# Performance work log

Hardware: AMD Instinct MI355X
Metric: run time of the kernel (lower is better)

## Reference

```python
import jax, jax.numpy as jnp
import numpy as np

B, NF, G, H, W = 4, 64, 8, 96, 96
K, KK = 3, 9
CG = NF // G  # channels per deformable group


def _conv3(x, w, b):
    # 3x3 conv, stride 1, pad 1, NCHW/OIHW
    y = jax.lax.conv_general_dilated(x, w, (1, 1), ((1, 1), (1, 1)),
                                     dimension_numbers=('NCHW', 'OIHW', 'NCHW'))
    return y + b[None, :, None, None]


def _lrelu(x):
    return jnp.where(x >= 0, x, 0.1 * x)


def _up2(x):
    # bilinear x2 upsample, align_corners=False (PyTorch semantics: src clamped at 0, indices clamped at n-1)
    def up_axis(x, axis):
        n = x.shape[axis]
        src = jnp.maximum((jnp.arange(2 * n, dtype=jnp.float32) + 0.5) / 2.0 - 0.5, 0.0)
        i0 = jnp.floor(src).astype(jnp.int32)
        i1 = jnp.minimum(i0 + 1, n - 1)
        t = (src - i0.astype(jnp.float32))
        x0 = jnp.take(x, i0, axis=axis)
        x1 = jnp.take(x, i1, axis=axis)
        shp = [1] * x.ndim
        shp[axis] = 2 * n
        t = t.reshape(shp)
        return x0 * (1.0 - t) + x1 * t
    return up_axis(up_axis(x, 2), 3)


def _dcn(x, off_feat, w_om, b_om, w_d, b_d):
    # Modulated deformable conv (DCNv2, separate offset input), 3x3, stride 1, pad 1, dil 1,
    # conv groups = 1, deformable groups = G.
    b, c, h, w = x.shape
    om = _conv3(off_feat, w_om, b_om)                     # [B, 3*G*KK, H, W]
    o_y, o_x, m = jnp.split(om, 3, axis=1)                # each [B, G*KK, H, W]
    off_y = o_y.reshape(b, G, KK, h, w)
    off_x = o_x.reshape(b, G, KK, h, w)
    mask = jax.nn.sigmoid(m).reshape(b, G, KK, h, w)

    dy = (jnp.arange(KK, dtype=jnp.float32) // K - 1.0)   # [-1,-1,-1,0,0,0,1,1,1]
    dx = (jnp.arange(KK, dtype=jnp.float32) % K - 1.0)
    ys = jnp.arange(h, dtype=jnp.float32)
    xs = jnp.arange(w, dtype=jnp.float32)
    # sampling positions: [B, G, KK, H, W]
    py = off_y + ys[None, None, None, :, None] + dy[None, None, :, None, None]
    px = off_x + xs[None, None, None, None, :] + dx[None, None, :, None, None]

    y0f = jnp.floor(py); x0f = jnp.floor(px)
    ty = py - y0f; tx = px - x0f
    y0 = y0f.astype(jnp.int32); x0 = x0f.astype(jnp.int32)
    y1 = y0 + 1; x1 = x0 + 1

    xg = x.reshape(b, G, CG, h * w)  # per-deformable-group channels

    def samp(iy, ix):
        valid = ((iy >= 0) & (iy < h) & (ix >= 0) & (ix < w)).astype(x.dtype)  # [B,G,KK,H,W]
        idx = jnp.clip(iy, 0, h - 1) * w + jnp.clip(ix, 0, w - 1)
        idxf = idx.reshape(b, G, 1, KK * h * w)
        v = jnp.take_along_axis(xg, jnp.broadcast_to(idxf, (b, G, CG, KK * h * w)), axis=3)
        return v.reshape(b, G, CG, KK, h, w) * valid[:, :, None]

    w00 = ((1 - ty) * (1 - tx))[:, :, None]
    w01 = ((1 - ty) * tx)[:, :, None]
    w10 = (ty * (1 - tx))[:, :, None]
    w11 = (ty * tx)[:, :, None]
    cols = (samp(y0, x0) * w00 + samp(y0, x1) * w01 +
            samp(y1, x0) * w10 + samp(y1, x1) * w11)
    cols = cols * mask[:, :, None]                        # modulation
    cols = cols.reshape(b, c, KK, h, w)
    out = jnp.einsum('bckhw,ock->bohw', cols, w_d.reshape(c, c, KK))
    return out + b_d[None, :, None, None]


def setup_inputs() -> dict:
    key = jax.random.key(0)
    ks = jax.random.split(key, 20)
    s = 0.05
    inp = {
        'src0': jax.random.normal(ks[0], (B, NF, H, W), jnp.float32),
        'src1': jax.random.normal(ks[1], (B, NF, H, W), jnp.float32),
        'last_offset': jax.random.normal(ks[2], (B, NF, H // 2, W // 2), jnp.float32),
        'last_feature': jax.random.normal(ks[3], (B, NF, H // 2, W // 2), jnp.float32),
        'w_off1': jax.random.normal(ks[4], (NF, 2 * NF, 3, 3), jnp.float32) * s,
        'b_off1': jax.random.normal(ks[5], (NF,), jnp.float32) * s,
        'w_off2': jax.random.normal(ks[6], (NF, 2 * NF, 3, 3), jnp.float32) * s,
        'b_off2': jax.random.normal(ks[7], (NF,), jnp.float32) * s,
        'w_off3': jax.random.normal(ks[8], (NF, NF, 3, 3), jnp.float32) * s,
        'b_off3': jax.random.normal(ks[9], (NF,), jnp.float32) * s,
        'w_om': jax.random.normal(ks[10], (3 * G * KK, NF, 3, 3), jnp.float32) * s,
        'b_om': jax.random.normal(ks[11], (3 * G * KK,), jnp.float32) * s,
        'w_dcn': jax.random.normal(ks[12], (NF, NF, 3, 3), jnp.float32) * s,
        'b_dcn': jax.random.normal(ks[13], (NF,), jnp.float32) * s,
        'w_fea': jax.random.normal(ks[14], (NF, 2 * NF, 3, 3), jnp.float32) * s,
        'b_fea': jax.random.normal(ks[15], (NF,), jnp.float32) * s,
    }
    return inp


def reference(src0, src1, last_offset, last_feature,
              w_off1, b_off1, w_off2, b_off2, w_off3, b_off3,
              w_om, b_om, w_dcn, b_dcn, w_fea, b_fea):
    offset = _lrelu(_conv3(jnp.concatenate([src0, src1], axis=1), w_off1, b_off1))
    lo = _up2(last_offset)
    offset = _lrelu(_conv3(jnp.concatenate([offset, lo * 2.0], axis=1), w_off2, b_off2))
    offset = _lrelu(_conv3(offset, w_off3, b_off3))
    feature = _dcn(src0, offset, w_om, b_om, w_dcn, b_dcn)
    lf = _up2(last_feature)
    feature = _conv3(jnp.concatenate([feature, lf], axis=1), w_fea, b_fea)
    feature = _lrelu(feature)
    return (offset, feature)
```

## Files before the change

### kernel.cpp

```cpp
#include <hip/hip_runtime.h>
#include <hip/hip_fp16.h>
#include <math.h>

typedef __attribute__((ext_vector_type(8))) short bf16x8;
typedef __attribute__((ext_vector_type(8))) _Float16 half8;
typedef __attribute__((ext_vector_type(4))) float f32x4;
typedef __attribute__((ext_vector_type(4))) int int4v;

#define GL_LDS16(g, l) __builtin_amdgcn_global_load_lds( \
    (const __attribute__((address_space(1))) void*)(g), \
    (__attribute__((address_space(3))) void*)(l), 16, 0, 0)

__device__ __forceinline__ ushort f2bf(float f) {
    union { float f; unsigned u; } v; v.f = f;
    unsigned r = (v.u + 0x7fffu + ((v.u >> 16) & 1u)) >> 16;
    return (ushort)r;
}
__device__ __forceinline__ float bf2f(ushort h) {
    union { unsigned u; float f; } v; v.u = ((unsigned)h) << 16;
    return v.f;
}

__device__ __forceinline__ void prep_one(const float* __restrict__ w,
        ushort* __restrict__ wp, int u, int Cin, int CoutR, int CoutP) {
    int oc = u % CoutP; int t = u / CoutP;
    int kg = t & 3; t >>= 2;
    int kk = t % 9; int cc = t / 9;
    alignas(16) ushort tmp[8];
    for (int j = 0; j < 8; ++j) {
        int c = cc * 32 + kg * 8 + j;
        float v = (oc < CoutR) ? w[((size_t)oc * Cin + c) * 9 + kk] : 0.f;
        tmp[j] = f2bf(v);
    }
    *(int4v*)(wp + (size_t)u * 8) = *(int4v*)tmp;
}

__global__ __launch_bounds__(256) void pack_combo_k(
        const float* __restrict__ s0, const float* __restrict__ s1,
        const float* __restrict__ lo, const float* __restrict__ lf,
        const float* __restrict__ w1, const float* __restrict__ w2,
        const float* __restrict__ w3, const float* __restrict__ wom,
        const float* __restrict__ wd, const float* __restrict__ wf,
        const float* __restrict__ bom,
        ushort* __restrict__ xin1, ushort* __restrict__ xin2,
        ushort* __restrict__ xin4, ushort* __restrict__ xg1,
        ushort* __restrict__ w1p, ushort* __restrict__ w2p,
        ushort* __restrict__ w3p, ushort* __restrict__ womp,
        ushort* __restrict__ wdp, ushort* __restrict__ wfp,
        float* __restrict__ bpp, float* __restrict__ zg) {
    int b = blockIdx.y;
    int z = blockIdx.z;
    int px = blockIdx.x * 64 + (threadIdx.x & 63);
    int u = threadIdx.x >> 6;
    if (z == 0) {
        for (int half = 0; half < 2; ++half) {
            int cg = u + half * 4;
            float vals[16];
            alignas(16) ushort tmp[16];
            for (int i = 0; i < 16; ++i) {
                int c = cg * 16 + i;
                float v = (c < 64) ? s0[((size_t)(b * 64 + c)) * 9216 + px]
                                   : s1[((size_t)(b * 64 + c - 64)) * 9216 + px];
                vals[i] = v;
                tmp[i] = f2bf(v);
            }
            ushort* dst = xin1 + ((size_t)(b * 9216) + px) * 128 + cg * 16;
            *(int4v*)dst = *(int4v*)&tmp[0];
            *(int4v*)(dst + 8) = *(int4v*)&tmp[8];
            if (half == 0) {
                alignas(16) __half th[16];
                for (int i = 0; i < 16; ++i) th[i] = __float2half(vals[i]);
                ushort* gdst = xg1 + (((size_t)(b * 8 + cg * 2) * 9216) + px) * 8;
                *(int4v*)gdst = *(int4v*)&th[0];
                *(int4v*)(gdst + 9216 * 8) = *(int4v*)&th[8];
            }
        }
    } else if (z < 3) {
        const float* in = (z == 1) ? lo : lf;
        float scale = (z == 1) ? 2.0f : 1.0f;
        ushort* xo = (z == 1) ? xin2 : xin4;
        int y = px / 96, x = px % 96;
        float sy = fmaxf(y * 0.5f - 0.25f, 0.f);
        float sx = fmaxf(x * 0.5f - 0.25f, 0.f);
        int y0 = (int)sy, x0 = (int)sx;
        float ty = sy - (float)y0, tx = sx - (float)x0;
        int y1 = min(y0 + 1, 47), x1 = min(x0 + 1, 47);
        alignas(16) ushort tmp[16];
        for (int i = 0; i < 16; ++i) {
            int c = u * 16 + i;
            const float* p = in + ((size_t)(b * 64 + c)) * 2304;
            float v00 = p[y0 * 48 + x0], v01 = p[y0 * 48 + x1];
            float v10 = p[y1 * 48 + x0], v11 = p[y1 * 48 + x1];
            float v = (v00 * (1.f - tx) + v01 * tx) * (1.f - ty)
                    + (v10 * (1.f - tx) + v11 * tx) * ty;
            tmp[i] = f2bf(v * scale);
        }
        ushort* dst = xo + ((size_t)(b * 9216) + px) * 128 + 64 + u * 16;
        *(int4v*)dst = *(int4v*)&tmp[0];
        *(int4v*)(dst + 8) = *(int4v*)&tmp[8];
    } else {
        int uu = (blockIdx.x + 144 * blockIdx.y) * 256 + threadIdx.x;
        if (uu < 9216) prep_one(w1, w1p, uu, 128, 64, 64);
        else if (uu < 18432) prep_one(w2, w2p, uu - 9216, 128, 64, 64);
        else if (uu < 23040) prep_one(w3, w3p, uu - 18432, 64, 64, 64);
        else if (uu < 43776) {
            int v = uu - 23040;
            int ocp = v % 288; int t = v / 288;
            int kg = t & 3; t >>= 2;
            int kk = t % 9; int cc = t / 9;
            int t3 = ocp & 3, gkkp = ocp >> 2;
            alignas(16) ushort tmp[8];
            for (int j = 0; j < 8; ++j) {
                int c = cc * 32 + kg * 8 + j;
                float vv = (t3 < 3)
                    ? wom[((size_t)(t3 * 72 + gkkp) * 64 + c) * 9 + kk] : 0.f;
                tmp[j] = f2bf(vv);
            }
            *(int4v*)(womp + (size_t)v * 8) = *(int4v*)tmp;
        } else if (uu < 48384) {
            int v = uu - 43776;
            int oc = v & 63; int gkk = v >> 6;
            int g = gkk / 9, kk = gkk % 9;
            alignas(16) __half tmp[8];
            for (int j = 0; j < 8; ++j)
                tmp[j] = __float2half(wd[((size_t)oc * 64 + g * 8 + j) * 9 + kk]);
            *(int4v*)(wdp + (size_t)v * 8) = *(int4v*)tmp;
        } else if (uu < 57600) prep_one(wf, wfp, uu - 48384, 128, 64, 64);
        else if (uu < 57888) {
            int ocp = uu - 57600; int t3 = ocp & 3, gkkp = ocp >> 2;
            bpp[ocp] = (t3 < 3) ? bom[t3 * 72 + gkkp] : 0.f;
        } else if (uu < 57904) zg[uu - 57888] = 0.f;
    }
}

template<int CIN, int MT, int NZ, bool LRELU, bool ST_F32, bool ST_CHL>
__global__ __launch_bounds__(256, 4) void conv_mfma_k(
        const ushort* __restrict__ xin,
        const ushort* __restrict__ wp,
        const float* __restrict__ bias,
        float* __restrict__ outf,
        ushort* __restrict__ chl,
        const ushort* __restrict__ zg,
        int CoutR, int CoutP, int ochs, int ocoff) {
    constexpr int SL = CIN / 64;
    constexpr int OCN = MT * 16;
    __shared__ ushort s_act[SL][7200];

    int tid = threadIdx.x;
    int wv = tid >> 6, ln = tid & 63;
    int l15 = ln & 15, l4 = ln >> 4;

    constexpr int TOTAL = 144 * 4 * NZ;
    constexpr int CHUNK = TOTAL / 8;
    int bid = blockIdx.x;
    int nid = (bid & 7) * CHUNK + (bid >> 3);
    int zc = nid % NZ; int r1 = nid / NZ;
    int tile = r1 % 144; int b = r1 / 144;
    int bx = (tile % 12) * 8, by = (tile / 12) * 8;
    int oc0 = zc * OCN;

    int px_l = wv * 16 + l15;
    int py = px_l >> 3, pxx = px_l & 7;
    int b_base = (py * 10 + pxx) * 72 + l4 * 8;

    const ushort* wlane = wp + ((size_t)l4 * CoutP + oc0 + l15) * 8;

    f32x4 acc[MT];
#pragma unroll
    for (int mt = 0; mt < MT; ++mt) acc[mt] = (f32x4){0.f, 0.f, 0.f, 0.f};

    auto STAGE = [&](int sl, int buf) {
        for (int i = tid; i < 900; i += 256) {
            int p = i / 9, q = i - p * 9;
            int gy = by + (p / 10) - 1, gx = bx + (p % 10) - 1;
            const ushort* src = zg;
            if (q < 8 && (unsigned)gy < 96u && (unsigned)gx < 96u)
                src = xin + ((size_t)(b * 9216 + gy * 96 + gx) * CIN
                             + sl * 64 + q * 8);
            GL_LDS16(src, s_act[buf] + (size_t)i * 8);
        }
    };

    STAGE(0, 0);
    __syncthreads();
#pragma unroll
    for (int sl = 0; sl < SL; ++sl) {
        if (sl + 1 < SL) STAGE(sl + 1, (sl + 1) & 1);
#pragma unroll
        for (int cc2 = 0; cc2 < 2; ++cc2) {
#pragma unroll
            for (int kk = 0; kk < 9; ++kk) {
                bf16x8 bfrag = *(const bf16x8*)(s_act[sl & (SL - 1)] + b_base +
                                   ((kk / 3) * 10 + (kk % 3)) * 72 + cc2 * 32);
#pragma unroll
                for (int mt = 0; mt < MT; ++mt) {
                    bf16x8 af = *(const bf16x8*)(wlane +
                        ((size_t)((sl * 2 + cc2) * 36 + kk * 4) * CoutP + mt * 16) * 8);
                    acc[mt] = __builtin_amdgcn_mfma_f32_16x16x32_bf16(
                        af, bfrag, acc[mt], 0, 0, 0);
                }
            }
        }
        if (sl + 1 < SL) __syncthreads();
    }

    int gy = by + py, gx = bx + pxx;
    size_t pxg = (size_t)b * 9216 + gy * 96 + gx;
#pragma unroll
    for (int mt = 0; mt < MT; ++mt) {
        int ocb = oc0 + mt * 16 + l4 * 4;
        ushort hb[4];
#pragma unroll
        for (int r = 0; r < 4; ++r) {
            int oc = ocb + r;
            float v = acc[mt][r] + ((oc < CoutR) ? bias[oc] : 0.f);
            if (LRELU) v = (v >= 0.f) ? v : 0.1f * v;
            hb[r] = f2bf(v);
            if (ST_F32 && oc < CoutR)
                outf[((size_t)b * CoutR + oc) * 9216 + gy * 96 + gx] = v;
        }
        if (ST_CHL && ocb < CoutR) {
            uint2 pk;
            pk.x = (uint)hb[0] | ((uint)hb[1] << 16);
            pk.y = (uint)hb[2] | ((uint)hb[3] << 16);
            *(uint2*)(chl + pxg * ochs + ocoff + ocb) = pk;
        }
    }
}

__global__ __launch_bounds__(192, 2) void dcn_fused_k(
        const ushort* __restrict__ xoff,
        const ushort* __restrict__ xg1,
        const ushort* __restrict__ womp,
        const float* __restrict__ bpp,
        const ushort* __restrict__ wdp,
        const float* __restrict__ bd, ushort* __restrict__ chl,
        const ushort* __restrict__ zg) {
    __shared__ ushort s_x[3456];
    __shared__ float s_red[2][64][17];
    int tid = threadIdx.x;
    int kq = tid >> 6, ln = tid & 63;
    int l15 = ln & 15, l4 = ln >> 4;
    int bid = blockIdx.x;
    int nid = (bid & 7) * 288 + (bid >> 3);
    int pxb = nid % 576; int b = nid / 576;
    int px0 = pxb * 16;
    int px = px0 + l15;
    int y = px0 / 96, x0 = px0 % 96;
    int xx = x0 + l15;

    for (int i = tid; i < 432; i += 192) {
        int P = i >> 3, s8 = i & 7;
        int q = s8 ^ (P & 7);
        int ry = y - 1 + P / 18, rx = x0 - 1 + P % 18;
        const ushort* src = zg;
        if ((unsigned)ry < 96u && (unsigned)rx < 96u)
            src = xoff + (((size_t)b * 9216 + ry * 96 + rx) * 64 + q * 8);
        GL_LDS16(src, s_x + (size_t)i * 8);
    }
    __syncthreads();

    f32x4 acc[4];
#pragma unroll
    for (int mt = 0; mt < 4; ++mt) acc[mt] = (f32x4){0.f, 0.f, 0.f, 0.f};

    int4v Ab[3][4];
    float cwb[3][4];

    auto PREP = [&](int s, const f32x4& aom, int4v* A, float* cw) {
        int st = kq * 6 + s;
        int gkk = st * 4 + l4;
        int g = gkk / 9, kk = gkk - g * 9;
        int bofs = st * 16 + l4 * 4;
        float oy = aom[0] + bpp[bofs];
        float ox = aom[1] + bpp[bofs + 1];
        float mm = 1.f / (1.f + __expf(-(aom[2] + bpp[bofs + 2])));
        float py = oy + (float)(y + kk / 3 - 1);
        float pxf = ox + (float)(xx + kk % 3 - 1);
        float yf = floorf(py), xf = floorf(pxf);
        float fy = py - yf, fx = pxf - xf;
        int iy0 = (int)yf, ix0 = (int)xf;
        int iy1 = iy0 + 1, ix1 = ix0 + 1;
        float vy0 = ((unsigned)iy0 < 96u) ? 1.f : 0.f;
        float vy1 = ((unsigned)iy1 < 96u) ? 1.f : 0.f;
        float vx0 = ((unsigned)ix0 < 96u) ? 1.f : 0.f;
        float vx1 = ((unsigned)ix1 < 96u) ? 1.f : 0.f;
        int r0 = min(max(iy0, 0), 95), r1 = min(max(iy1, 0), 95);
        int lb = min(max(ix0, 0), 94);
        float h0 = (float)min(max(ix0 - lb, 0), 1);
        float h1 = (float)min(max(ix1 - lb, 0), 1);
        float wx0 = (1.f - fx) * vx0, wx1 = fx * vx1;
        float xw0 = wx0 * (1.f - h0) + wx1 * (1.f - h1);
        float xw1 = wx0 * h0 + wx1 * h1;
        float rw0 = (1.f - fy) * vy0 * mm, rw1 = fy * vy1 * mm;
        cw[0] = rw0 * xw0; cw[1] = rw0 * xw1;
        cw[2] = rw1 * xw0; cw[3] = rw1 * xw1;
        const ushort* gp = xg1 + ((size_t)(b * 8 + g) * 9216) * 8;
        const ushort* p0 = gp + ((size_t)(r0 * 96 + lb)) * 8;
        const ushort* p1 = gp + ((size_t)(r1 * 96 + lb)) * 8;
        A[0] = *(const int4v*)p0;
        A[1] = *(const int4v*)(p0 + 8);
        A[2] = *(const int4v*)p1;
        A[3] = *(const int4v*)(p1 + 8);
    };

    auto CONSUME = [&](int s, const int4v* A, const float* cw) {
        union { int4v v; __half2 h2[4]; } a0, a1, b0, b1;
        a0.v = A[0]; a1.v = A[1]; b0.v = A[2]; b1.v = A[3];
        __half2 w0 = __float2half2_rn(cw[0]);
        __half2 w1 = __float2half2_rn(cw[1]);
        __half2 w2 = __float2half2_rn(cw[2]);
        __half2 w3 = __float2half2_rn(cw[3]);
        union { __half2 h2[4]; half8 v; } bu;
#pragma unroll
        for (int j = 0; j < 4; ++j) {
            __half2 t = __hmul2(a0.h2[j], w0);
            t = __hfma2(a1.h2[j], w1, t);
            t = __hfma2(b0.h2[j], w2, t);
            t = __hfma2(b1.h2[j], w3, t);
            bu.h2[j] = t;
        }
        int gkk = (kq * 6 + s) * 4 + l4;
#pragma unroll
        for (int mt = 0; mt < 4; ++mt) {
            half8 af = *(const half8*)(wdp +
                ((size_t)gkk * 64 + mt * 16 + l15) * 8);
            acc[mt] = __builtin_amdgcn_mfma_f32_16x16x32_f16(
                af, bu.v, acc[mt], 0, 0, 0);
        }
    };

#pragma unroll
    for (int s = 0; s < 8; ++s) {
        if (s < 6) {
            f32x4 aom = (f32x4){0.f, 0.f, 0.f, 0.f};
#pragma unroll
            for (int kk = 0; kk < 9; ++kk) {
                int ky = kk / 3, kx = kk % 3;
#pragma unroll
                for (int cc = 0; cc < 2; ++cc) {
                    int P = ky * 18 + l15 + kx;
                    int c8 = cc * 4 + l4;
                    bf16x8 bfrag = *(const bf16x8*)(s_x +
                        ((size_t)(P * 8 + (c8 ^ (P & 7)))) * 8);
                    bf16x8 af = *(const bf16x8*)(womp +
                        ((size_t)(((cc * 9 + kk) * 4 + l4) * 288)
                         + (kq * 6 + s) * 16 + l15) * 8);
                    aom = __builtin_amdgcn_mfma_f32_16x16x32_bf16(
                        af, bfrag, aom, 0, 0, 0);
                }
            }
            PREP(s, aom, Ab[s % 3], cwb[s % 3]);
        }
        if (s >= 2) CONSUME(s - 2, Ab[(s - 2) % 3], cwb[(s - 2) % 3]);
    }

    if (kq) {
#pragma unroll
        for (int mt = 0; mt < 4; ++mt)
#pragma unroll
            for (int r = 0; r < 4; ++r)
                s_red[kq - 1][ln][mt * 4 + r] = acc[mt][r];
    }
    __syncthreads();
    if (!kq) {
        size_t pb = (size_t)b * 9216 + px;
#pragma unroll
        for (int mt = 0; mt < 4; ++mt) {
            ushort hb[4];
#pragma unroll
            for (int r = 0; r < 4; ++r) {
                int oc = mt * 16 + l4 * 4 + r;
                float v = acc[mt][r] + s_red[0][ln][mt * 4 + r]
                        + s_red[1][ln][mt * 4 + r] + bd[oc];
                hb[r] = f2bf(v);
            }
            uint2 pk;
            pk.x = (uint)hb[0] | ((uint)hb[1] << 16);
            pk.y = (uint)hb[2] | ((uint)hb[3] << 16);
            *(uint2*)(chl + pb * 128 + mt * 16 + l4 * 4) = pk;
        }
    }
}

extern "C" void kernel_launch(void* const* d_in, const int* in_sizes, int n_in,
                              void* d_out, int out_size, void* d_ws, size_t ws_size,
                              hipStream_t stream) {
    const float* src0  = (const float*)d_in[0];
    const float* src1  = (const float*)d_in[1];
    const float* l_off = (const float*)d_in[2];
    const float* l_fea = (const float*)d_in[3];
    const float* w1 = (const float*)d_in[4];   const float* b1 = (const float*)d_in[5];
    const float* w2 = (const float*)d_in[6];   const float* b2 = (const float*)d_in[7];
    const float* w3 = (const float*)d_in[8];   const float* b3 = (const float*)d_in[9];
    const float* wom = (const float*)d_in[10]; const float* bom = (const float*)d_in[11];
    const float* wd = (const float*)d_in[12];  const float* bd = (const float*)d_in[13];
    const float* wf = (const float*)d_in[14];  const float* bf = (const float*)d_in[15];

    char* W = (char*)d_ws;
    ushort* xin1 = (ushort*)(W + 0);
    ushort* xin2 = (ushort*)(W + 9437184);
    ushort* xoff = (ushort*)(W + 9437184);
    ushort* xin3 = (ushort*)(W + 18874368);
    ushort* xin4 = (ushort*)(W + 44826624);
    ushort* xg1  = (ushort*)(W + 54263808);
    ushort* w1p  = (ushort*)(W + 58982400);
    ushort* w2p  = (ushort*)(W + 59129856);
    ushort* w3p  = (ushort*)(W + 59277312);
    ushort* womp = (ushort*)(W + 59351040);
    ushort* wdp  = (ushort*)(W + 59682816);
    ushort* wfp  = (ushort*)(W + 59756544);
    float*  bpp  = (float*)(W + 59904000);
    float*  zgrd = (float*)(W + 59905152);

    float* out_off = (float*)d_out;
    float* out_fea = out_off + (size_t)4 * 64 * 9216;

    pack_combo_k<<<dim3(144, 4, 4), 256, 0, stream>>>(
        src0, src1, l_off, l_fea, w1, w2, w3, wom, wd, wf, bom,
        xin1, xin2, xin4, xg1, w1p, w2p, w3p, womp, wdp, wfp, bpp, zgrd);

    const ushort* zg = (const ushort*)zgrd;
    conv_mfma_k<128, 2, 2, true, false, true><<<1152, 256, 0, stream>>>(
        xin1, w1p, b1, nullptr, xin2, zg, 64, 64, 128, 0);
    conv_mfma_k<128, 2, 2, true, false, true><<<1152, 256, 0, stream>>>(
        xin2, w2p, b2, nullptr, xin3, zg, 64, 64, 64, 0);
    conv_mfma_k<64, 2, 2, true, true, true><<<1152, 256, 0, stream>>>(
        xin3, w3p, b3, out_off, xoff, zg, 64, 64, 64, 0);
    dcn_fused_k<<<2304, 192, 0, stream>>>(xoff, xg1, womp, bpp, wdp, bd,
                                          xin4, zg);
    conv_mfma_k<128, 2, 2, true, true, false><<<1152, 256, 0, stream>>>(
        xin4, wfp, bf, out_fea, nullptr, zg, 64, 64, 0, 0);
}
```

Baseline: 131.9 us.

## Process two 16-pixel groups per block in fused DCN kernel

Each block of the fused offset-conv plus deformable-conv kernel now covers 32 pixels instead of 16, with a wider shared-memory halo tile and a halved grid. The offset-mask and DCN weight fragments loaded from global memory are reused across two MFMA accumulator sets, which halves weight traffic per pixel and amortizes halo loads. The software pipeline changes from a 3-deep to a 2-deep buffer. This raises register and LDS use per block and may reduce occupancy or latency hiding.

```diff
diff --git a/kernel.cpp b/kernel.cpp
--- a/kernel.cpp
+++ b/kernel.cpp
@@ -236,23 +236,21 @@
         const ushort* __restrict__ wdp,
         const float* __restrict__ bd, ushort* __restrict__ chl,
         const ushort* __restrict__ zg) {
-    __shared__ ushort s_x[3456];
-    __shared__ float s_red[2][64][17];
+    __shared__ ushort s_x[816 * 8];
+    __shared__ float s_red[2][2][64][17];
     int tid = threadIdx.x;
     int kq = tid >> 6, ln = tid & 63;
     int l15 = ln & 15, l4 = ln >> 4;
     int bid = blockIdx.x;
-    int nid = (bid & 7) * 288 + (bid >> 3);
-    int pxb = nid % 576; int b = nid / 576;
-    int px0 = pxb * 16;
-    int px = px0 + l15;
+    int nid = (bid & 7) * 144 + (bid >> 3);
+    int pxb = nid % 288; int b = nid / 288;
+    int px0 = pxb * 32;
     int y = px0 / 96, x0 = px0 % 96;
-    int xx = x0 + l15;
-
-    for (int i = tid; i < 432; i += 192) {
+
+    for (int i = tid; i < 816; i += 192) {
         int P = i >> 3, s8 = i & 7;
         int q = s8 ^ (P & 7);
-        int ry = y - 1 + P / 18, rx = x0 - 1 + P % 18;
+        int ry = y - 1 + P / 34, rx = x0 - 1 + P % 34;
         const ushort* src = zg;
         if ((unsigned)ry < 96u && (unsigned)rx < 96u)
             src = xoff + (((size_t)b * 9216 + ry * 96 + rx) * 64 + q * 8);
@@ -260,18 +258,22 @@
     }
     __syncthreads();
 
-    f32x4 acc[4];
-#pragma unroll
-    for (int mt = 0; mt < 4; ++mt) acc[mt] = (f32x4){0.f, 0.f, 0.f, 0.f};
-
-    int4v Ab[3][4];
-    float cwb[3][4];
-
-    auto PREP = [&](int s, const f32x4& aom, int4v* A, float* cw) {
+    f32x4 acc0[4], acc1[4];
+#pragma unroll
+    for (int mt = 0; mt < 4; ++mt) {
+        acc0[mt] = (f32x4){0.f, 0.f, 0.f, 0.f};
+        acc1[mt] = (f32x4){0.f, 0.f, 0.f, 0.f};
+    }
+
+    int4v Ab[2][2][4];
+    float cwb[2][2][4];
+
+    auto PREP = [&](int s, int gx, const f32x4& aom, int4v* A, float* cw) {
         int st = kq * 6 + s;
         int gkk = st * 4 + l4;
         int g = gkk / 9, kk = gkk - g * 9;
         int bofs = st * 16 + l4 * 4;
+        int xx = x0 + gx * 16 + l15;
         float oy = aom[0] + bpp[bofs];
         float ox = aom[1] + bpp[bofs + 1];
         float mm = 1.f / (1.f + __expf(-(aom[2] + bpp[bofs + 2])));
@@ -304,7 +306,7 @@
         A[3] = *(const int4v*)(p1 + 8);
     };
 
-    auto CONSUME = [&](int s, const int4v* A, const float* cw) {
+    auto LERP = [&](const int4v* A, const float* cw, half8* out) {
         union { int4v v; __half2 h2[4]; } a0, a1, b0, b1;
         a0.v = A[0]; a1.v = A[1]; b0.v = A[2]; b1.v = A[3];
         __half2 w0 = __float2half2_rn(cw[0]);
@@ -320,65 +322,86 @@
             t = __hfma2(b1.h2[j], w3, t);
             bu.h2[j] = t;
         }
+        *out = bu.v;
+    };
+
+    auto CONSUME2 = [&](int s, int par) {
+        half8 bu0, bu1;
+        LERP(Ab[par][0], cwb[par][0], &bu0);
+        LERP(Ab[par][1], cwb[par][1], &bu1);
         int gkk = (kq * 6 + s) * 4 + l4;
 #pragma unroll
         for (int mt = 0; mt < 4; ++mt) {
             half8 af = *(const half8*)(wdp +
                 ((size_t)gkk * 64 + mt * 16 + l15) * 8);
-            acc[mt] = __builtin_amdgcn_mfma_f32_16x16x32_f16(
-                af, bu.v, acc[mt], 0, 0, 0);
+            acc0[mt] = __builtin_amdgcn_mfma_f32_16x16x32_f16(
+                af, bu0, acc0[mt], 0, 0, 0);
+            acc1[mt] = __builtin_amdgcn_mfma_f32_16x16x32_f16(
+                af, bu1, acc1[mt], 0, 0, 0);
         }
     };
 
 #pragma unroll
-    for (int s = 0; s < 8; ++s) {
-        if (s < 6) {
-            f32x4 aom = (f32x4){0.f, 0.f, 0.f, 0.f};
-#pragma unroll
-            for (int kk = 0; kk < 9; ++kk) {
-                int ky = kk / 3, kx = kk % 3;
-#pragma unroll
-                for (int cc = 0; cc < 2; ++cc) {
-                    int P = ky * 18 + l15 + kx;
-                    int c8 = cc * 4 + l4;
-                    bf16x8 bfrag = *(const bf16x8*)(s_x +
-                        ((size_t)(P * 8 + (c8 ^ (P & 7)))) * 8);
-                    bf16x8 af = *(const bf16x8*)(womp +
-                        ((size_t)(((cc * 9 + kk) * 4 + l4) * 288)
-                         + (kq * 6 + s) * 16 + l15) * 8);
-                    aom = __builtin_amdgcn_mfma_f32_16x16x32_bf16(
-                        af, bfrag, aom, 0, 0, 0);
-                }
-            }
-            PREP(s, aom, Ab[s % 3], cwb[s % 3]);
-        }
-        if (s >= 2) CONSUME(s - 2, Ab[(s - 2) % 3], cwb[(s - 2) % 3]);
-    }
+    for (int s = 0; s < 6; ++s) {
+        f32x4 aom0 = (f32x4){0.f, 0.f, 0.f, 0.f};
+        f32x4 aom1 = (f32x4){0.f, 0.f, 0.f, 0.f};
+#pragma unroll
+        for (int kk = 0; kk < 9; ++kk) {
+            int ky = kk / 3, kx = kk % 3;
+#pragma unroll
+            for (int cc = 0; cc < 2; ++cc) {
+                int c8 = cc * 4 + l4;
+                int P0 = ky * 34 + l15 + kx;
+                int P1 = P0 + 16;
+                bf16x8 bf0 = *(const bf16x8*)(s_x +
+                    ((size_t)(P0 * 8 + (c8 ^ (P0 & 7)))) * 8);
+                bf16x8 bf1 = *(const bf16x8*)(s_x +
+                    ((size_t)(P1 * 8 + (c8 ^ (P1 & 7)))) * 8);
+                bf16x8 af = *(const bf16x8*)(womp +
+                    ((size_t)(((cc * 9 + kk) * 4 + l4) * 288)
+                     + (kq * 6 + s) * 16 + l15) * 8);
+                aom0 = __builtin_amdgcn_mfma_f32_16x16x32_bf16(
+                    af, bf0, aom0, 0, 0, 0);
+                aom1 = __builtin_amdgcn_mfma_f32_16x16x32_bf16(
+                    af, bf1, aom1, 0, 0, 0);
+            }
+        }
+        PREP(s, 0, aom0, Ab[s & 1][0], cwb[s & 1][0]);
+        PREP(s, 1, aom1, Ab[s & 1][1], cwb[s & 1][1]);
+        if (s >= 1) CONSUME2(s - 1, (s - 1) & 1);
+    }
+    CONSUME2(5, 1);
 
     if (kq) {
 #pragma unroll
         for (int mt = 0; mt < 4; ++mt)
 #pragma unroll
-            for (int r = 0; r < 4; ++r)
-                s_red[kq - 1][ln][mt * 4 + r] = acc[mt][r];
+            for (int r = 0; r < 4; ++r) {
+                s_red[kq - 1][0][ln][mt * 4 + r] = acc0[mt][r];
+                s_red[kq - 1][1][ln][mt * 4 + r] = acc1[mt][r];
+            }
     }
     __syncthreads();
     if (!kq) {
-        size_t pb = (size_t)b * 9216 + px;
-#pragma unroll
-        for (int mt = 0; mt < 4; ++mt) {
-            ushort hb[4];
-#pragma unroll
-            for (int r = 0; r < 4; ++r) {
-                int oc = mt * 16 + l4 * 4 + r;
-                float v = acc[mt][r] + s_red[0][ln][mt * 4 + r]
-                        + s_red[1][ln][mt * 4 + r] + bd[oc];
-                hb[r] = f2bf(v);
-            }
-            uint2 pk;
-            pk.x = (uint)hb[0] | ((uint)hb[1] << 16);
-            pk.y = (uint)hb[2] | ((uint)hb[3] << 16);
-            *(uint2*)(chl + pb * 128 + mt * 16 + l4 * 4) = pk;
+#pragma unroll
+        for (int gx = 0; gx < 2; ++gx) {
+            size_t pb = (size_t)b * 9216 + px0 + gx * 16 + l15;
+#pragma unroll
+            for (int mt = 0; mt < 4; ++mt) {
+                ushort hb[4];
+#pragma unroll
+                for (int r = 0; r < 4; ++r) {
+                    int oc = mt * 16 + l4 * 4 + r;
+                    float a = gx ? acc1[mt][r] : acc0[mt][r];
+                    float v = a + s_red[0][gx][ln][mt * 4 + r]
+                            + s_red[1][gx][ln][mt * 4 + r] + bd[oc];
+                    hb[r] = f2bf(v);
+                }
+                uint2 pk;
+                pk.x = (uint)hb[0] | ((uint)hb[1] << 16);
+                pk.y = (uint)hb[2] | ((uint)hb[3] << 16);
+                *(uint2*)(chl + pb * 128 + mt * 16 + l4 * 4) = pk;
+            }
         }
     }
 }
@@ -427,7 +450,7 @@
         xin2, w2p, b2, nullptr, xin3, zg, 64, 64, 64, 0);
     conv_mfma_k<64, 2, 2, true, true, true><<<1152, 256, 0, stream>>>(
         xin3, w3p, b3, out_off, xoff, zg, 64, 64, 64, 0);
-    dcn_fused_k<<<2304, 192, 0, stream>>>(xoff, xg1, womp, bpp, wdp, bd,
+    dcn_fused_k<<<1152, 192, 0, stream>>>(xoff, xg1, womp, bpp, wdp, bd,
                                           xin4, zg);
     conv_mfma_k<128, 2, 2, true, true, false><<<1152, 256, 0, stream>>>(
         xin4, wfp, bf, out_fea, nullptr, zg, 64, 64, 0, 0);
```

Result: slower. 205.3 us (+55.6%).
